# Kernel tuning notes

Measured on AMD Instinct MI355X. Metric: run time of the kernel, lower is better.

Reference implementation:

```python
import jax, jax.numpy as jnp
import numpy as np

SCALE = 2
EPS = 1e-5  # BatchNorm2d default eps


def conv1x1(x, W, b):
    # x: [B,C,H,W], W: [O,C], b: [O]
    return jnp.einsum('bchw,oc->bohw', x, W) + b[None, :, None, None]


def maxpool(x, s):
    B, C, H, W = x.shape
    return x.reshape(B, C, H // s, s, W // s, s).max(axis=(3, 5))


def upsample_bilinear_ac(x, s):
    # bilinear upsample, align_corners=True
    B, C, H, W = x.shape
    Ho, Wo = H * s, W * s
    ys = jnp.arange(Ho) * ((H - 1) / (Ho - 1))
    xs = jnp.arange(Wo) * ((W - 1) / (Wo - 1))
    y0 = jnp.floor(ys).astype(jnp.int32)
    y1 = jnp.minimum(y0 + 1, H - 1)
    wy = (ys - y0).astype(x.dtype)
    x0 = jnp.floor(xs).astype(jnp.int32)
    x1 = jnp.minimum(x0 + 1, W - 1)
    wx = (xs - x0).astype(x.dtype)
    rows = x[:, :, y0, :] * (1 - wy)[None, None, :, None] + x[:, :, y1, :] * wy[None, None, :, None]
    return rows[:, :, :, x0] * (1 - wx) + rows[:, :, :, x1] * wx


def setup_inputs() -> dict:
    key = jax.random.key(0)
    ks = jax.random.split(key, 9)
    B, Cin, Cm, dk, H, W = 4, 64, 64, 64, 128, 128
    return {
        'x': jax.random.normal(ks[0], (B, Cin, H, W), jnp.float32),
        'memory': jax.random.normal(ks[1], (B, Cm, H, W), jnp.float32),
        'W_qkv': jax.random.normal(ks[2], (3 * dk, Cm), jnp.float32) * 0.05,
        'b_qkv': jax.random.normal(ks[3], (3 * dk,), jnp.float32) * 0.05,
        'W_out': jax.random.normal(ks[4], (Cin, dk), jnp.float32) * 0.05,
        'b_out': jax.random.normal(ks[5], (Cin,), jnp.float32) * 0.05,
        'bn_gamma': jax.random.uniform(ks[6], (Cin,), jnp.float32, 0.5, 1.5),
        'bn_beta': jax.random.normal(ks[7], (Cin,), jnp.float32) * 0.05,
        'gamma': jax.random.normal(ks[8], (1,), jnp.float32) * 0.1,
    }


def reference(x, memory, W_qkv, b_qkv, W_out, b_out, bn_gamma, bn_beta, gamma):
    d_k = W_qkv.shape[0] // 3
    qkv = conv1x1(memory, W_qkv, b_qkv)
    qkv = maxpool(qkv, SCALE)
    q, k, v = jnp.split(qkv, 3, axis=1)
    B, C, H, W = v.shape
    q = q.reshape(B, C, H * W).transpose(0, 2, 1)  # [B,N,C]
    k = k.reshape(B, C, H * W)                      # [B,C,N]
    v = v.reshape(B, C, H * W).transpose(0, 2, 1)   # [B,N,C]
    scale = jnp.asarray(d_k, x.dtype) ** 0.5
    attn = jax.nn.softmax(jnp.einsum('bnc,bcm->bnm', q, k) / scale, axis=-1)
    S = jnp.einsum('bnm,bmc->bnc', attn, v).transpose(0, 2, 1).reshape(B, C, H, W)
    S = upsample_bilinear_ac(S, SCALE)
    S = conv1x1(S, W_out, b_out)
    # BatchNorm2d (training mode: biased batch stats over B,H,W)
    mean = S.mean(axis=(0, 2, 3), keepdims=True)
    var = S.var(axis=(0, 2, 3), keepdims=True)
    S = (S - mean) / jnp.sqrt(var + EPS) * bn_gamma[None, :, None, None] + bn_beta[None, :, None, None]
    return x + gamma[0] * S
```

## Files before the change

### kernel.cpp

```cpp
#include <hip/hip_runtime.h>
#include <stdint.h>

typedef unsigned short u16;
typedef unsigned int   u32;
typedef __attribute__((ext_vector_type(8))) __bf16 bf16x8;
typedef __attribute__((ext_vector_type(4))) float  f32x4;
typedef __attribute__((ext_vector_type(2))) float  f32x2;
typedef __attribute__((ext_vector_type(4))) u32    u32x4;
typedef __attribute__((ext_vector_type(2))) u32    u32x2;

#define QSCALE 0.18033688011112042f

__device__ __forceinline__ u16 f2bf(float x) {
  u32 u = __builtin_bit_cast(u32, x);
  u = (u + 0x7FFFu + ((u >> 16) & 1u)) >> 16;
  return (u16)u;
}

__device__ __forceinline__ u32 cvt_pk_bf16(float lo, float hi) {
  u32 r;
  asm("v_cvt_pk_bf16_f32 %0, %1, %2" : "=v"(r) : "v"(lo), "v"(hi));
  return r;
}

__global__ __launch_bounds__(256) void k_qkvpool(
    const float* __restrict__ mem, const float* __restrict__ Wqkv,
    const float* __restrict__ bqkv, u16* __restrict__ Q,
    u16* __restrict__ K, u16* __restrict__ V)
{
  const int oy = blockIdx.x, b = blockIdx.y, t = threadIdx.x;
  const int w = t >> 6, l4 = t & 15, lh = (t >> 4) & 3;

  __shared__ __align__(16) u16 lds[40960];
  u16* mlds = lds;
  u16* wlds = lds + 16384;
  u16* qlds = lds + 28672;
  u16* klds = lds + 32768;
  u16* vlds = lds + 36864;

  float bias[3][4];
  #pragma unroll
  for (int j = 0; j < 3; ++j)
    #pragma unroll
    for (int r = 0; r < 4; ++r) {
      int oc = w * 48 + 16 * j + lh * 4 + r;
      float bv = bqkv[oc];
      bias[j][r] = (oc < 64) ? bv * QSCALE : bv;
    }

  {
    const float* src = mem + ((size_t)b * 64) * 16384 + 2 * oy * 128;
    const int pxl = t & 63, cqh = t >> 6;
    #pragma unroll
    for (int i = 0; i < 16; ++i) {
      int px = pxl + 64 * (i & 3);
      int c0 = (cqh + 4 * (i >> 2)) * 4;
      float f0 = src[(size_t)(c0 + 0) * 16384 + px];
      float f1 = src[(size_t)(c0 + 1) * 16384 + px];
      float f2 = src[(size_t)(c0 + 2) * 16384 + px];
      float f3 = src[(size_t)(c0 + 3) * 16384 + px];
      u32x2 pk;
      pk[0] = (u32)f2bf(f0) | ((u32)f2bf(f1) << 16);
      pk[1] = (u32)f2bf(f2) | ((u32)f2bf(f3) << 16);
      *(u32x2*)(mlds + px * 64 + (((c0 * 2) ^ ((px & 7) << 4)) >> 1)) = pk;
    }
  }
  {
    #pragma unroll
    for (int i = 0; i < 12; ++i) {
      int chunk = t + 256 * i;
      int oc = chunk >> 4, c0 = (chunk & 15) * 4;
      f32x4 wv = *(const f32x4*)(Wqkv + oc * 64 + c0);
      u32x2 pk;
      pk[0] = (u32)f2bf(wv[0]) | ((u32)f2bf(wv[1]) << 16);
      pk[1] = (u32)f2bf(wv[2]) | ((u32)f2bf(wv[3]) << 16);
      *(u32x2*)(wlds + oc * 64 + (((c0 * 2) ^ ((oc & 7) << 4)) >> 1)) = pk;
    }
  }
  __syncthreads();

  const int sw  = (l4 & 7) << 4;
  const int oF0 = ((lh * 16) ^ sw) >> 1;
  const int oF1 = ((64 + lh * 16) ^ sw) >> 1;
  bf16x8 af[3][2];
  #pragma unroll
  for (int j = 0; j < 3; ++j) {
    const u16* ar = wlds + (w * 48 + 16 * j + l4) * 64;
    af[j][0] = *(const bf16x8*)(ar + oF0);
    af[j][1] = *(const bf16x8*)(ar + oF1);
  }

  #pragma unroll 2
  for (int tp = 0; tp < 8; ++tp) {
    const u16* br0 = mlds + (16 * tp + l4) * 64;
    const u16* br1 = mlds + (128 + 16 * tp + l4) * 64;
    bf16x8 b00 = *(const bf16x8*)(br0 + oF0);
    bf16x8 b01 = *(const bf16x8*)(br0 + oF1);
    bf16x8 b10 = *(const bf16x8*)(br1 + oF0);
    bf16x8 b11 = *(const bf16x8*)(br1 + oF1);
    const int ox = 8 * tp + (l4 >> 1);
    #pragma unroll
    for (int j = 0; j < 3; ++j) {
      f32x4 a0 = {0, 0, 0, 0}, a1 = {0, 0, 0, 0};
      a0 = __builtin_amdgcn_mfma_f32_16x16x32_bf16(af[j][0], b00, a0, 0, 0, 0);
      a0 = __builtin_amdgcn_mfma_f32_16x16x32_bf16(af[j][1], b01, a0, 0, 0, 0);
      a1 = __builtin_amdgcn_mfma_f32_16x16x32_bf16(af[j][0], b10, a1, 0, 0, 0);
      a1 = __builtin_amdgcn_mfma_f32_16x16x32_bf16(af[j][1], b11, a1, 0, 0, 0);
      const int ocj = w * 48 + 16 * j;
      const float sc = (ocj < 64) ? QSCALE : 1.0f;
      #pragma unroll
      for (int r = 0; r < 4; ++r) {
        float m = fmaxf(a0[r], a1[r]);
        m = fmaxf(m, __shfl_xor(m, 1, 64));
        u16 val = f2bf(m * sc + bias[j][r]);
        if ((l4 & 1) == 0) {
          int oc = ocj + lh * 4 + r;
          if (ocj < 64)       qlds[ox * 64 + oc]          = val;
          else if (ocj < 128) klds[ox * 64 + (oc - 64)]   = val;
          else                vlds[(oc - 128) * 64 + ox]  = val;
        }
      }
    }
  }
  __syncthreads();

  #pragma unroll
  for (int i = 0; i < 2; ++i) {
    int f = t + 256 * i;
    int r = f >> 3, e8 = (f & 7) * 8;
    size_t nb = (size_t)oy * 64;
    *(u32x4*)(Q + ((size_t)b * 4096 + nb + r) * 64 + e8) = *(const u32x4*)(qlds + r * 64 + e8);
    *(u32x4*)(K + ((size_t)b * 4096 + nb + r) * 64 + e8) = *(const u32x4*)(klds + r * 64 + e8);
    *(u32x4*)(V + ((size_t)b * 64 + r) * 4096 + nb + e8) = *(const u32x4*)(vlds + r * 64 + e8);
  }
}

__global__ __launch_bounds__(1024, 4) void k_attn(
    const u16* __restrict__ Q, const u16* __restrict__ K,
    const u16* __restrict__ V, float* __restrict__ Sa)
{
  const int qb = blockIdx.x, b = blockIdx.y, t = threadIdx.x;
  const int w = t >> 6, l4 = t & 15, lh = (t >> 4) & 3;
  const int sgrp = w >> 2, wq = w & 3;

  __shared__ __align__(16) u16 kvbuf[16384 + 18432];

  u16* kt_w = kvbuf + sgrp * 4096;
  u16* vt_w = kvbuf + 16384 + sgrp * 4608;

  const int qrow = qb * 64 + wq * 16 + l4;
  const u16* qp = Q + ((size_t)b * 4096 + qrow) * 64 + lh * 8;
  bf16x8 qa0 = *(const bf16x8*)qp;
  bf16x8 qa1 = *(const bf16x8*)(qp + 32);

  f32x4 ot[4] = {{0,0,0,0},{0,0,0,0},{0,0,0,0},{0,0,0,0}};
  float lr = 0.f;

  const int tl = t & 255;
  const int skr = tl >> 2, skc = tl & 3;
  const u16* kgp = K + ((size_t)b * 4096 + sgrp * 1024 + skr) * 64 + skc * 16;
  const u16* vgp = V + ((size_t)b * 64 + skr) * 4096 + sgrp * 1024 + skc * 16;
  const u32 fbw = (u32)(((skr & 3) | (((skr >> 3) & 1) << 2)) << 4);
  u16* kwp0 = kt_w + skr * 64 + ((((u32)(skc * 32))      ^ fbw) >> 1);
  u16* kwp1 = kt_w + skr * 64 + ((((u32)(skc * 32 + 16)) ^ fbw) >> 1);
  u16* vwp  = vt_w + skr * 72 + skc * 16;

  const int rbase = ((l4 >> 2) << 3) + (l4 & 3);
  const int fbr   = ((l4 & 3) | (((l4 >> 2) & 1) << 2)) << 4;
  const int offL  = ((lh * 16) ^ fbr) >> 1;
  const int offH  = offL ^ 32;

  u32x4 rk0 = *(const u32x4*)kgp;
  u32x4 rk1 = *(const u32x4*)(kgp + 8);
  u32x4 rv0 = *(const u32x4*)vgp;
  u32x4 rv1 = *(const u32x4*)(vgp + 8);

  #pragma unroll 1
  for (int kti = 0; kti < 16; ++kti) {
    *(u32x4*)kwp0 = rk0;
    *(u32x4*)kwp1 = rk1;
    *(u32x4*)vwp = rv0;
    *(u32x4*)(vwp + 8) = rv1;
    __syncthreads();

    if (kti < 15) {
      rk0 = *(const u32x4*)(kgp + (kti + 1) * 4096);
      rk1 = *(const u32x4*)(kgp + (kti + 1) * 4096 + 8);
      rv0 = *(const u32x4*)(vgp + (kti + 1) * 64);
      rv1 = *(const u32x4*)(vgp + (kti + 1) * 64 + 8);
    }

    #pragma unroll
    for (int ss = 0; ss < 2; ++ss) {
      const u16* kr0 = kt_w + (ss * 32 + rbase) * 64;
      const u16* kr1 = kr0 + 4 * 64;
      bf16x8 vf0 = *(const bf16x8*)(vt_w + (l4)      * 72 + ss * 32 + lh * 8);
      bf16x8 vf1 = *(const bf16x8*)(vt_w + (16 + l4) * 72 + ss * 32 + lh * 8);
      bf16x8 vf2 = *(const bf16x8*)(vt_w + (32 + l4) * 72 + ss * 32 + lh * 8);
      bf16x8 vf3 = *(const bf16x8*)(vt_w + (48 + l4) * 72 + ss * 32 + lh * 8);
      bf16x8 k00 = *(const bf16x8*)(kr0 + offL);
      bf16x8 k01 = *(const bf16x8*)(kr0 + offH);
      bf16x8 k10 = *(const bf16x8*)(kr1 + offL);
      bf16x8 k11 = *(const bf16x8*)(kr1 + offH);

      f32x4 s0 = {0, 0, 0, 0}, s1 = {0, 0, 0, 0};
      s0 = __builtin_amdgcn_mfma_f32_16x16x32_bf16(k00, qa0, s0, 0, 0, 0);
      s0 = __builtin_amdgcn_mfma_f32_16x16x32_bf16(k01, qa1, s0, 0, 0, 0);
      s1 = __builtin_amdgcn_mfma_f32_16x16x32_bf16(k10, qa0, s1, 0, 0, 0);
      s1 = __builtin_amdgcn_mfma_f32_16x16x32_bf16(k11, qa1, s1, 0, 0, 0);

      float p0[4], p1[4];
      #pragma unroll
      for (int r = 0; r < 4; ++r) {
        p0[r] = exp2f(s0[r]);
        p1[r] = exp2f(s1[r]);
        lr += p0[r] + p1[r];
      }
      u32x4 pw;
      pw[0] = cvt_pk_bf16(p0[0], p0[1]);
      pw[1] = cvt_pk_bf16(p0[2], p0[3]);
      pw[2] = cvt_pk_bf16(p1[0], p1[1]);
      pw[3] = cvt_pk_bf16(p1[2], p1[3]);
      bf16x8 pf = __builtin_bit_cast(bf16x8, pw);

      ot[0] = __builtin_amdgcn_mfma_f32_16x16x32_bf16(vf0, pf, ot[0], 0, 0, 0);
      ot[1] = __builtin_amdgcn_mfma_f32_16x16x32_bf16(vf1, pf, ot[1], 0, 0, 0);
      ot[2] = __builtin_amdgcn_mfma_f32_16x16x32_bf16(vf2, pf, ot[2], 0, 0, 0);
      ot[3] = __builtin_amdgcn_mfma_f32_16x16x32_bf16(vf3, pf, ot[3], 0, 0, 0);
    }
    __syncthreads();
  }

  lr += __shfl_xor(lr, 16, 64);
  lr += __shfl_xor(lr, 32, 64);

  float* opb = (float*)kvbuf;
  float* mlb = (float*)(kvbuf + 32768);
  #pragma unroll
  for (int d = 0; d < 4; ++d)
    #pragma unroll
    for (int r = 0; r < 4; ++r)
      opb[w * 1024 + (16 * d + lh * 4 + r) * 16 + l4] = ot[d][r];
  if (lh == 0) mlb[w * 16 + l4] = lr;
  __syncthreads();

  const int ch = t >> 4, q0v = (t & 15) * 4;
  f32x4 res;
  #pragma unroll
  for (int j = 0; j < 4; ++j) {
    int q = q0v + j, wq2 = q >> 4, ql = q & 15;
    float L = mlb[(wq2)*16      + ql] + mlb[(4 + wq2)*16  + ql]
            + mlb[(8 + wq2)*16  + ql] + mlb[(12 + wq2)*16 + ql];
    float O = opb[(wq2)*1024      + ch * 16 + ql]
            + opb[(4 + wq2)*1024  + ch * 16 + ql]
            + opb[(8 + wq2)*1024  + ch * 16 + ql]
            + opb[(12 + wq2)*1024 + ch * 16 + ql];
    res[j] = O / L;
  }
  *(f32x4*)(Sa + ((size_t)b * 64 + ch) * 4096 + (size_t)qb * 64 + q0v) = res;
}

__global__ __launch_bounds__(256) void k_wout(
    const float* __restrict__ Sa, const float* __restrict__ Wout,
    const float* __restrict__ bo, float* __restrict__ U, float* __restrict__ stats)
{
  const int nb = blockIdx.x, b = blockIdx.y, t = threadIdx.x;
  if (nb == 0 && b == 0 && t < 128) stats[t] = 0.f;
  __shared__ __align__(16) float st[64][64];
  __shared__ __align__(16) float wt[64][64];
  #pragma unroll
  for (int i = 0; i < 4; ++i) {
    int f = t + 256 * i;
    int c = f >> 4, n4 = (f & 15) * 4;
    *(f32x4*)&st[c][n4] = *(const f32x4*)(Sa + ((size_t)b * 64 + c) * 4096 + nb * 64 + n4);
  }
  #pragma unroll 4
  for (int i = 0; i < 16; ++i) {
    int f = t + 256 * i;
    wt[f & 63][f >> 6] = Wout[f];
  }
  __syncthreads();
  const int n = t & 63, og = t >> 6;
  float acc[16];
  #pragma unroll
  for (int j = 0; j < 16; ++j) acc[j] = 0.f;
  #pragma unroll 2
  for (int c = 0; c < 64; ++c) {
    float sv = st[c][n];
    f32x4 w0 = *(const f32x4*)&wt[c][og * 16];
    f32x4 w1 = *(const f32x4*)&wt[c][og * 16 + 4];
    f32x4 w2 = *(const f32x4*)&wt[c][og * 16 + 8];
    f32x4 w3 = *(const f32x4*)&wt[c][og * 16 + 12];
    #pragma unroll
    for (int j = 0; j < 4; ++j) {
      acc[j]      += w0[j] * sv;
      acc[4 + j]  += w1[j] * sv;
      acc[8 + j]  += w2[j] * sv;
      acc[12 + j] += w3[j] * sv;
    }
  }
  #pragma unroll
  for (int j = 0; j < 16; ++j) {
    int oc = og * 16 + j;
    U[((size_t)b * 64 + oc) * 4096 + (size_t)nb * 64 + n] = acc[j] + bo[oc];
  }
}

__global__ __launch_bounds__(256) void k_stats(const float* __restrict__ U,
                                               float* __restrict__ stats)
{
  const int c = blockIdx.x & 63, b = blockIdx.x >> 6, t = threadIdx.x;
  __shared__ __align__(16) float up[4096];
  __shared__ float red[8];
  #pragma unroll
  for (int i = 0; i < 4; ++i) {
    int f = t + 256 * i;
    *(f32x4*)&up[f * 4] = *(const f32x4*)(U + ((size_t)b * 64 + c) * 4096 + f * 4);
  }
  __syncthreads();
  const float R = 0.49606299212598425f;
  float sum = 0.f, ssq = 0.f;
  for (int i = 0; i < 64; ++i) {
    int px = t + 256 * i;
    int yo = px >> 7, xo = px & 127;
    float ys = yo * R; int y0 = (int)ys; float wy = ys - y0; int y1 = min(y0 + 1, 63);
    float xs = xo * R; int x0 = (int)xs; float wx = xs - x0; int x1 = min(x0 + 1, 63);
    const float* r0 = up + y0 * 64; const float* r1 = up + y1 * 64;
    float v0 = r0[x0] * (1.f - wx) + r0[x1] * wx;
    float v1 = r1[x0] * (1.f - wx) + r1[x1] * wx;
    float v = v0 * (1.f - wy) + v1 * wy;
    sum += v; ssq += v * v;
  }
  #pragma unroll
  for (int d = 32; d >= 1; d >>= 1) {
    sum += __shfl_down(sum, d, 64);
    ssq += __shfl_down(ssq, d, 64);
  }
  if ((t & 63) == 0) { red[t >> 6] = sum; red[4 + (t >> 6)] = ssq; }
  __syncthreads();
  if (t == 0) {
    atomicAdd(&stats[c],      red[0] + red[1] + red[2] + red[3]);
    atomicAdd(&stats[64 + c], red[4] + red[5] + red[6] + red[7]);
  }
}

__global__ __launch_bounds__(256) void k_apply(
    const float* __restrict__ U, const float* __restrict__ stats,
    const float* __restrict__ x, const float* __restrict__ bng,
    const float* __restrict__ bnb, const float* __restrict__ gam,
    float* __restrict__ out)
{
  const int c = blockIdx.x & 63, b = blockIdx.x >> 6, t = threadIdx.x;
  __shared__ __align__(16) float up[4096];
  #pragma unroll
  for (int i = 0; i < 4; ++i) {
    int f = t + 256 * i;
    *(f32x4*)&up[f * 4] = *(const f32x4*)(U + ((size_t)b * 64 + c) * 4096 + f * 4);
  }
  __syncthreads();
  const float inv = 1.0f / 65536.0f;
  float mean = stats[c] * inv;
  float var  = stats[64 + c] * inv - mean * mean;
  float rsig = rsqrtf(var + 1e-5f);
  float g = gam[0];
  float A  = g * bng[c] * rsig;
  float Bc = g * (bnb[c] - mean * rsig * bng[c]);
  const float R = 0.49606299212598425f;
  const size_t base = ((size_t)b * 64 + c) * 16384;
  for (int i = 0; i < 64; ++i) {
    int px = t + 256 * i;
    int yo = px >> 7, xo = px & 127;
    float ys = yo * R; int y0 = (int)ys; float wy = ys - y0; int y1 = min(y0 + 1, 63);
    float xs = xo * R; int x0 = (int)xs; float wx = xs - x0; int x1 = min(x0 + 1, 63);
    const float* r0 = up + y0 * 64; const float* r1 = up + y1 * 64;
    float v0 = r0[x0] * (1.f - wx) + r0[x1] * wx;
    float v1 = r1[x0] * (1.f - wx) + r1[x1] * wx;
    float v = v0 * (1.f - wy) + v1 * wy;
    out[base + px] = x[base + px] + v * A + Bc;
  }
}

extern "C" void kernel_launch(void* const* d_in, const int* in_sizes, int n_in,
                              void* d_out, int out_size, void* d_ws, size_t ws_size,
                              hipStream_t stream)
{
  const float* x      = (const float*)d_in[0];
  const float* memory = (const float*)d_in[1];
  const float* Wqkv   = (const float*)d_in[2];
  const float* bqkv   = (const float*)d_in[3];
  const float* Wout   = (const float*)d_in[4];
  const float* bout   = (const float*)d_in[5];
  const float* bng    = (const float*)d_in[6];
  const float* bnb    = (const float*)d_in[7];
  const float* gamma  = (const float*)d_in[8];

  char* ws = (char*)d_ws;
  u16*   Q     = (u16*)(ws + 0);
  u16*   Kk    = (u16*)(ws + (2u << 20));
  u16*   Vt    = (u16*)(ws + (4u << 20));
  float* Satt  = (float*)(ws + (6u << 20));
  float* U     = (float*)(ws + (10u << 20));
  float* stats = (float*)(ws + (14u << 20));
  float* out   = (float*)d_out;

  k_qkvpool<<<dim3(64, 4), 256, 0, stream>>>(memory, Wqkv, bqkv, Q, Kk, Vt);
  k_attn   <<<dim3(64, 4), 1024, 0, stream>>>(Q, Kk, Vt, Satt);
  k_wout   <<<dim3(64, 4), 256, 0, stream>>>(Satt, Wout, bout, U, stats);
  k_stats  <<<256, 256, 0, stream>>>(U, stats);
  k_apply  <<<256, 256, 0, stream>>>(U, stats, x, bng, bnb, gamma, out);
}
```

Before: 76.26 us.

## Fold W_out projection into V before attention and drop k_wout kernel

Since softmax rows sum to one and the output conv is linear, the W_out projection is applied to pooled V inside the QKV kernel (MFMA on a transposed V tile), and b_out is added in the attention epilogue. This removes the separate k_wout kernel and its round trip through the intermediate buffer. The qkvpool kernel moves to 512 threads, and the stats/apply kernels move to 1024 threads with fewer loop iterations. The change adds an extra bf16 rounding of the projected V, which may slightly alter accuracy.

```diff
diff --git a/kernel.cpp b/kernel.cpp
--- a/kernel.cpp
+++ b/kernel.cpp
@@ -23,38 +23,43 @@
   return r;
 }
 
-__global__ __launch_bounds__(256) void k_qkvpool(
+__global__ __launch_bounds__(512) void k_qkvpool(
     const float* __restrict__ mem, const float* __restrict__ Wqkv,
-    const float* __restrict__ bqkv, u16* __restrict__ Q,
-    u16* __restrict__ K, u16* __restrict__ V)
+    const float* __restrict__ bqkv, const float* __restrict__ Wout,
+    u16* __restrict__ Q, u16* __restrict__ K, u16* __restrict__ V,
+    float* __restrict__ stats)
 {
   const int oy = blockIdx.x, b = blockIdx.y, t = threadIdx.x;
   const int w = t >> 6, l4 = t & 15, lh = (t >> 4) & 3;
-
-  __shared__ __align__(16) u16 lds[40960];
-  u16* mlds = lds;
-  u16* wlds = lds + 16384;
-  u16* qlds = lds + 28672;
-  u16* klds = lds + 32768;
-  u16* vlds = lds + 36864;
+  const int wq = w & 3, wp = w >> 2;
+
+  if (oy == 0 && b == 0 && t < 128) stats[t] = 0.f;
+
+  __shared__ __align__(16) u16 lds[49152];
+  u16* mlds  = lds;
+  u16* wlds  = lds + 16384;
+  u16* qlds  = lds + 28672;
+  u16* klds  = lds + 32768;
+  u16* vldsT = lds + 36864;
+  u16* wolds = lds + 40960;
+  u16* vplds = lds + 45056;
 
   float bias[3][4];
   #pragma unroll
   for (int j = 0; j < 3; ++j)
     #pragma unroll
     for (int r = 0; r < 4; ++r) {
-      int oc = w * 48 + 16 * j + lh * 4 + r;
+      int oc = wq * 48 + 16 * j + lh * 4 + r;
       float bv = bqkv[oc];
       bias[j][r] = (oc < 64) ? bv * QSCALE : bv;
     }
 
   {
     const float* src = mem + ((size_t)b * 64) * 16384 + 2 * oy * 128;
-    const int pxl = t & 63, cqh = t >> 6;
-    #pragma unroll
-    for (int i = 0; i < 16; ++i) {
-      int px = pxl + 64 * (i & 3);
-      int c0 = (cqh + 4 * (i >> 2)) * 4;
+    #pragma unroll
+    for (int i = 0; i < 8; ++i) {
+      int g = t + 512 * i;
+      int px = g & 255, c0 = (g >> 8) * 4;
       float f0 = src[(size_t)(c0 + 0) * 16384 + px];
       float f1 = src[(size_t)(c0 + 1) * 16384 + px];
       float f2 = src[(size_t)(c0 + 2) * 16384 + px];
@@ -67,14 +72,26 @@
   }
   {
     #pragma unroll
-    for (int i = 0; i < 12; ++i) {
-      int chunk = t + 256 * i;
-      int oc = chunk >> 4, c0 = (chunk & 15) * 4;
+    for (int i = 0; i < 6; ++i) {
+      int g = t + 512 * i;
+      int oc = g >> 4, c0 = (g & 15) * 4;
       f32x4 wv = *(const f32x4*)(Wqkv + oc * 64 + c0);
       u32x2 pk;
       pk[0] = (u32)f2bf(wv[0]) | ((u32)f2bf(wv[1]) << 16);
       pk[1] = (u32)f2bf(wv[2]) | ((u32)f2bf(wv[3]) << 16);
       *(u32x2*)(wlds + oc * 64 + (((c0 * 2) ^ ((oc & 7) << 4)) >> 1)) = pk;
+    }
+  }
+  {
+    #pragma unroll
+    for (int i = 0; i < 2; ++i) {
+      int g = t + 512 * i;
+      int oc = g >> 4, c0 = (g & 15) * 4;
+      f32x4 wv = *(const f32x4*)(Wout + oc * 64 + c0);
+      u32x2 pk;
+      pk[0] = (u32)f2bf(wv[0]) | ((u32)f2bf(wv[1]) << 16);
+      pk[1] = (u32)f2bf(wv[2]) | ((u32)f2bf(wv[3]) << 16);
+      *(u32x2*)(wolds + oc * 64 + (((c0 * 2) ^ ((oc & 7) << 4)) >> 1)) = pk;
     }
   }
   __syncthreads();
@@ -85,13 +102,14 @@
   bf16x8 af[3][2];
   #pragma unroll
   for (int j = 0; j < 3; ++j) {
-    const u16* ar = wlds + (w * 48 + 16 * j + l4) * 64;
+    const u16* ar = wlds + (wq * 48 + 16 * j + l4) * 64;
     af[j][0] = *(const bf16x8*)(ar + oF0);
     af[j][1] = *(const bf16x8*)(ar + oF1);
   }
 
   #pragma unroll 2
-  for (int tp = 0; tp < 8; ++tp) {
+  for (int tpi = 0; tpi < 4; ++tpi) {
+    const int tp = wp * 4 + tpi;
     const u16* br0 = mlds + (16 * tp + l4) * 64;
     const u16* br1 = mlds + (128 + 16 * tp + l4) * 64;
     bf16x8 b00 = *(const bf16x8*)(br0 + oF0);
@@ -106,7 +124,7 @@
       a0 = __builtin_amdgcn_mfma_f32_16x16x32_bf16(af[j][1], b01, a0, 0, 0, 0);
       a1 = __builtin_amdgcn_mfma_f32_16x16x32_bf16(af[j][0], b10, a1, 0, 0, 0);
       a1 = __builtin_amdgcn_mfma_f32_16x16x32_bf16(af[j][1], b11, a1, 0, 0, 0);
-      const int ocj = w * 48 + 16 * j;
+      const int ocj = wq * 48 + 16 * j;
       const float sc = (ocj < 64) ? QSCALE : 1.0f;
       #pragma unroll
       for (int r = 0; r < 4; ++r) {
@@ -115,29 +133,53 @@
         u16 val = f2bf(m * sc + bias[j][r]);
         if ((l4 & 1) == 0) {
           int oc = ocj + lh * 4 + r;
-          if (ocj < 64)       qlds[ox * 64 + oc]          = val;
-          else if (ocj < 128) klds[ox * 64 + (oc - 64)]   = val;
-          else                vlds[(oc - 128) * 64 + ox]  = val;
+          if (ocj < 64)       qlds[ox * 64 + oc]        = val;
+          else if (ocj < 128) klds[ox * 64 + (oc - 64)] = val;
+          else {
+            int vch = oc - 128;
+            vldsT[ox * 64 + (((vch * 2) ^ ((ox & 7) << 4)) >> 1)] = val;
+          }
         }
       }
     }
   }
   __syncthreads();
 
-  #pragma unroll
-  for (int i = 0; i < 2; ++i) {
-    int f = t + 256 * i;
-    int r = f >> 3, e8 = (f & 7) * 8;
+  {
+    const u16* ar = wolds + (wq * 16 + l4) * 64;
+    bf16x8 aw0 = *(const bf16x8*)(ar + oF0);
+    bf16x8 aw1 = *(const bf16x8*)(ar + oF1);
+    #pragma unroll
+    for (int nti = 0; nti < 2; ++nti) {
+      const int nt = wp * 2 + nti;
+      const u16* brow = vldsT + (nt * 16 + l4) * 64;
+      bf16x8 bw0 = *(const bf16x8*)(brow + oF0);
+      bf16x8 bw1 = *(const bf16x8*)(brow + oF1);
+      f32x4 u = {0, 0, 0, 0};
+      u = __builtin_amdgcn_mfma_f32_16x16x32_bf16(aw0, bw0, u, 0, 0, 0);
+      u = __builtin_amdgcn_mfma_f32_16x16x32_bf16(aw1, bw1, u, 0, 0, 0);
+      #pragma unroll
+      for (int r = 0; r < 4; ++r) {
+        int oc = wq * 16 + lh * 4 + r;
+        vplds[oc * 64 + nt * 16 + l4] = f2bf(u[r]);
+      }
+    }
+  }
+  __syncthreads();
+
+  {
+    int r = t >> 3, e8 = (t & 7) * 8;
     size_t nb = (size_t)oy * 64;
     *(u32x4*)(Q + ((size_t)b * 4096 + nb + r) * 64 + e8) = *(const u32x4*)(qlds + r * 64 + e8);
     *(u32x4*)(K + ((size_t)b * 4096 + nb + r) * 64 + e8) = *(const u32x4*)(klds + r * 64 + e8);
-    *(u32x4*)(V + ((size_t)b * 64 + r) * 4096 + nb + e8) = *(const u32x4*)(vlds + r * 64 + e8);
+    *(u32x4*)(V + ((size_t)b * 64 + r) * 4096 + nb + e8) = *(const u32x4*)(vplds + r * 64 + e8);
   }
 }
 
 __global__ __launch_bounds__(1024, 4) void k_attn(
     const u16* __restrict__ Q, const u16* __restrict__ K,
-    const u16* __restrict__ V, float* __restrict__ Sa)
+    const u16* __restrict__ V, const float* __restrict__ bo,
+    float* __restrict__ Sa)
 {
   const int qb = blockIdx.x, b = blockIdx.y, t = threadIdx.x;
   const int w = t >> 6, l4 = t & 15, lh = (t >> 4) & 3;
@@ -245,6 +287,7 @@
   __syncthreads();
 
   const int ch = t >> 4, q0v = (t & 15) * 4;
+  const float bout_c = bo[ch];
   f32x4 res;
   #pragma unroll
   for (int j = 0; j < 4; ++j) {
@@ -255,73 +298,24 @@
             + opb[(4 + wq2)*1024  + ch * 16 + ql]
             + opb[(8 + wq2)*1024  + ch * 16 + ql]
             + opb[(12 + wq2)*1024 + ch * 16 + ql];
-    res[j] = O / L;
+    res[j] = O / L + bout_c;
   }
   *(f32x4*)(Sa + ((size_t)b * 64 + ch) * 4096 + (size_t)qb * 64 + q0v) = res;
 }
 
-__global__ __launch_bounds__(256) void k_wout(
-    const float* __restrict__ Sa, const float* __restrict__ Wout,
-    const float* __restrict__ bo, float* __restrict__ U, float* __restrict__ stats)
-{
-  const int nb = blockIdx.x, b = blockIdx.y, t = threadIdx.x;
-  if (nb == 0 && b == 0 && t < 128) stats[t] = 0.f;
-  __shared__ __align__(16) float st[64][64];
-  __shared__ __align__(16) float wt[64][64];
-  #pragma unroll
-  for (int i = 0; i < 4; ++i) {
-    int f = t + 256 * i;
-    int c = f >> 4, n4 = (f & 15) * 4;
-    *(f32x4*)&st[c][n4] = *(const f32x4*)(Sa + ((size_t)b * 64 + c) * 4096 + nb * 64 + n4);
-  }
-  #pragma unroll 4
-  for (int i = 0; i < 16; ++i) {
-    int f = t + 256 * i;
-    wt[f & 63][f >> 6] = Wout[f];
-  }
-  __syncthreads();
-  const int n = t & 63, og = t >> 6;
-  float acc[16];
-  #pragma unroll
-  for (int j = 0; j < 16; ++j) acc[j] = 0.f;
-  #pragma unroll 2
-  for (int c = 0; c < 64; ++c) {
-    float sv = st[c][n];
-    f32x4 w0 = *(const f32x4*)&wt[c][og * 16];
-    f32x4 w1 = *(const f32x4*)&wt[c][og * 16 + 4];
-    f32x4 w2 = *(const f32x4*)&wt[c][og * 16 + 8];
-    f32x4 w3 = *(const f32x4*)&wt[c][og * 16 + 12];
-    #pragma unroll
-    for (int j = 0; j < 4; ++j) {
-      acc[j]      += w0[j] * sv;
-      acc[4 + j]  += w1[j] * sv;
-      acc[8 + j]  += w2[j] * sv;
-      acc[12 + j] += w3[j] * sv;
-    }
-  }
-  #pragma unroll
-  for (int j = 0; j < 16; ++j) {
-    int oc = og * 16 + j;
-    U[((size_t)b * 64 + oc) * 4096 + (size_t)nb * 64 + n] = acc[j] + bo[oc];
-  }
-}
-
-__global__ __launch_bounds__(256) void k_stats(const float* __restrict__ U,
-                                               float* __restrict__ stats)
+__global__ __launch_bounds__(1024) void k_stats(const float* __restrict__ U,
+                                                float* __restrict__ stats)
 {
   const int c = blockIdx.x & 63, b = blockIdx.x >> 6, t = threadIdx.x;
   __shared__ __align__(16) float up[4096];
-  __shared__ float red[8];
-  #pragma unroll
-  for (int i = 0; i < 4; ++i) {
-    int f = t + 256 * i;
-    *(f32x4*)&up[f * 4] = *(const f32x4*)(U + ((size_t)b * 64 + c) * 4096 + f * 4);
-  }
+  __shared__ float red[32];
+  *(f32x4*)&up[t * 4] = *(const f32x4*)(U + ((size_t)b * 64 + c) * 4096 + t * 4);
   __syncthreads();
   const float R = 0.49606299212598425f;
   float sum = 0.f, ssq = 0.f;
-  for (int i = 0; i < 64; ++i) {
-    int px = t + 256 * i;
+  #pragma unroll 4
+  for (int i = 0; i < 16; ++i) {
+    int px = t + 1024 * i;
     int yo = px >> 7, xo = px & 127;
     float ys = yo * R; int y0 = (int)ys; float wy = ys - y0; int y1 = min(y0 + 1, 63);
     float xs = xo * R; int x0 = (int)xs; float wx = xs - x0; int x1 = min(x0 + 1, 63);
@@ -336,15 +330,18 @@
     sum += __shfl_down(sum, d, 64);
     ssq += __shfl_down(ssq, d, 64);
   }
-  if ((t & 63) == 0) { red[t >> 6] = sum; red[4 + (t >> 6)] = ssq; }
+  if ((t & 63) == 0) { red[t >> 6] = sum; red[16 + (t >> 6)] = ssq; }
   __syncthreads();
   if (t == 0) {
-    atomicAdd(&stats[c],      red[0] + red[1] + red[2] + red[3]);
-    atomicAdd(&stats[64 + c], red[4] + red[5] + red[6] + red[7]);
-  }
-}
-
-__global__ __launch_bounds__(256) void k_apply(
+    float s = 0.f, q = 0.f;
+    #pragma unroll
+    for (int i = 0; i < 16; ++i) { s += red[i]; q += red[16 + i]; }
+    atomicAdd(&stats[c], s);
+    atomicAdd(&stats[64 + c], q);
+  }
+}
+
+__global__ __launch_bounds__(1024) void k_apply(
     const float* __restrict__ U, const float* __restrict__ stats,
     const float* __restrict__ x, const float* __restrict__ bng,
     const float* __restrict__ bnb, const float* __restrict__ gam,
@@ -352,11 +349,7 @@
 {
   const int c = blockIdx.x & 63, b = blockIdx.x >> 6, t = threadIdx.x;
   __shared__ __align__(16) float up[4096];
-  #pragma unroll
-  for (int i = 0; i < 4; ++i) {
-    int f = t + 256 * i;
-    *(f32x4*)&up[f * 4] = *(const f32x4*)(U + ((size_t)b * 64 + c) * 4096 + f * 4);
-  }
+  *(f32x4*)&up[t * 4] = *(const f32x4*)(U + ((size_t)b * 64 + c) * 4096 + t * 4);
   __syncthreads();
   const float inv = 1.0f / 65536.0f;
   float mean = stats[c] * inv;
@@ -367,8 +360,9 @@
   float Bc = g * (bnb[c] - mean * rsig * bng[c]);
   const float R = 0.49606299212598425f;
   const size_t base = ((size_t)b * 64 + c) * 16384;
-  for (int i = 0; i < 64; ++i) {
-    int px = t + 256 * i;
+  #pragma unroll 4
+  for (int i = 0; i < 16; ++i) {
+    int px = t + 1024 * i;
     int yo = px >> 7, xo = px & 127;
     float ys = yo * R; int y0 = (int)ys; float wy = ys - y0; int y1 = min(y0 + 1, 63);
     float xs = xo * R; int x0 = (int)xs; float wx = xs - x0; int x1 = min(x0 + 1, 63);
@@ -398,14 +392,12 @@
   u16*   Q     = (u16*)(ws + 0);
   u16*   Kk    = (u16*)(ws + (2u << 20));
   u16*   Vt    = (u16*)(ws + (4u << 20));
-  float* Satt  = (float*)(ws + (6u << 20));
   float* U     = (float*)(ws + (10u << 20));
   float* stats = (float*)(ws + (14u << 20));
   float* out   = (float*)d_out;
 
-  k_qkvpool<<<dim3(64, 4), 256, 0, stream>>>(memory, Wqkv, bqkv, Q, Kk, Vt);
-  k_attn   <<<dim3(64, 4), 1024, 0, stream>>>(Q, Kk, Vt, Satt);
-  k_wout   <<<dim3(64, 4), 256, 0, stream>>>(Satt, Wout, bout, U, stats);
-  k_stats  <<<256, 256, 0, stream>>>(U, stats);
-  k_apply  <<<256, 256, 0, stream>>>(U, stats, x, bng, bnb, gamma, out);
-}
+  k_qkvpool<<<dim3(64, 4), 512, 0, stream>>>(memory, Wqkv, bqkv, Wout, Q, Kk, Vt, stats);
+  k_attn   <<<dim3(64, 4), 1024, 0, stream>>>(Q, Kk, Vt, bout, U);
+  k_stats  <<<256, 1024, 0, stream>>>(U, stats);
+  k_apply  <<<256, 1024, 0, stream>>>(U, stats, x, bng, bnb, gamma, out);
+}
```

After: 61.71 us. 19.1% less time.
